# Optimization experiments

Measured on AMD Instinct MI355X. Metric: run time of the kernel, lower is better.

## Reference

```python
import jax, jax.numpy as jnp
import numpy as np

EPS = 0.01  # the module uses 1/sqrt(||x||^2 + 0.01) for cosine normalization


def setup_inputs() -> dict:
    key = jax.random.key(0)
    k1, k2, k3, k4, k5, k6 = jax.random.split(key, 6)
    B, L, L1, D = 512, 256, 256, 128
    sequence = jax.random.randint(k1, (B, L), 0, 10000, dtype=jnp.int32)
    last_sequence = jax.random.randint(k2, (B, L), 0, 2, dtype=jnp.int32)
    sequence_1 = jax.random.randint(k3, (B, L1), 0, 10000, dtype=jnp.int32)
    hist_1 = jax.random.normal(k4, (B, L, D), dtype=jnp.float32)
    hist_2 = jax.random.normal(k5, (B, L1, D), dtype=jnp.float32)
    W = jax.random.normal(k6, (D, D), dtype=jnp.float32) * (1.0 / np.sqrt(D))
    return {"sequence": sequence, "last_sequence": last_sequence,
            "sequence_1": sequence_1, "hist_1": hist_1, "hist_2": hist_2, "W": W}


def reference(sequence, last_sequence, sequence_1, hist_1, hist_2, W):
    # Masks: nonzero ids -> 1.0 (cast to bool then float in the original)
    m = (sequence != 0).astype(jnp.float32)        # [B, L]   key mask for self-attn
    m1 = (sequence_1 != 0).astype(jnp.float32)     # [B, L1]  key mask for cross-attn
    last = last_sequence.astype(jnp.float32)       # [B, L]   last-position indicator

    # --- self cosine-similarity attention over hist_1 ---
    # cos[b,i,j] = <hist_1[b,i], hist_1[b,j]> / (sqrt(||h_i||^2+eps) * sqrt(||h_j||^2+eps))
    dots = jnp.einsum('bid,bjd->bij', hist_1, hist_1)            # [B, L, L]
    inv = jax.lax.rsqrt(jnp.sum(hist_1 * hist_1, axis=-1) + EPS)  # [B, L]
    cos = dots * inv[:, :, None] * inv[:, None, :]
    # softmax-style weighting: exp(cos) masked over keys j (unnormalized exp, per original)
    w = jnp.exp(cos) * m[:, None, :]                             # [B, L, L]
    wsum = jnp.sum(w, axis=-1)                                   # [B, L]
    h_self = jnp.einsum('bij,bjd->bid', w, hist_1) / wsum[..., None]  # [B, L, D]

    # residual add, mask by query validity, then pool at the 'last' position
    h_all_add = (h_self + hist_1) * m[..., None]                 # [B, L, D]
    h_last = jnp.sum(h_all_add * last[..., None], axis=1)        # [B, D]

    # --- cross cosine-similarity attention: h_last attends over hist_2 ---
    dots2 = jnp.einsum('bkd,bd->bk', hist_2, h_last)             # [B, L1]
    inv2k = jax.lax.rsqrt(jnp.sum(hist_2 * hist_2, axis=-1) + EPS)  # [B, L1]
    inv2q = jax.lax.rsqrt(jnp.sum(h_last * h_last, axis=-1) + EPS)  # [B]
    cos2 = dots2 * inv2k * inv2q[:, None]
    w2 = jnp.exp(cos2) * m1                                      # [B, L1]
    h = jnp.einsum('bk,bkd->bd', w2, hist_2) / jnp.sum(w2, axis=-1, keepdims=True)

    out = jax.nn.relu(h @ W)                                     # [B, D]
    return out.reshape(-1, 1, W.shape[0])                        # [B, 1, hidden_num]
```

## Files before the change

### kernel.cpp

```cpp
#include <hip/hip_runtime.h>


using u16 = unsigned short;
using u32 = unsigned int;
typedef __attribute__((ext_vector_type(8))) short bf16x8;
typedef __attribute__((ext_vector_type(4))) float f32x4;
typedef __attribute__((ext_vector_type(4))) u32 u32x4;
typedef __attribute__((ext_vector_type(2))) u32 u32x2;

#define KST 136
#define TST 40
#define WSTR 40

__device__ __forceinline__ u16 f2bf(float f) {
  union { float f; u32 i; } v; v.f = f;
  u32 r = v.i + 0x7FFFu + ((v.i >> 16) & 1u);
  return (u16)(r >> 16);
}
__device__ __forceinline__ bf16x8 as_bf(u32x4 x) {
  union { u32x4 u; bf16x8 b; } c; c.u = x; return c.b;
}
__device__ __forceinline__ u32x4 pack_bf8(const float* p, float& ss) {
  const float4 a = *(const float4*)p;
  const float4 c = *(const float4*)(p + 4);
  ss += a.x*a.x + a.y*a.y + a.z*a.z + a.w*a.w
      + c.x*c.x + c.y*c.y + c.z*c.z + c.w*c.w;
  u32x4 v;
  v.x = (u32)f2bf(a.x) | ((u32)f2bf(a.y) << 16);
  v.y = (u32)f2bf(a.z) | ((u32)f2bf(a.w) << 16);
  v.z = (u32)f2bf(c.x) | ((u32)f2bf(c.y) << 16);
  v.w = (u32)f2bf(c.z) | ((u32)f2bf(c.w) << 16);
  return v;
}

__device__ __forceinline__ void stage_tile(u32x4 v, float ss, u16* kb, u16* tb,
                                           float* invt, int wv, int q, int m16) {
  const int row = wv * 4 + q;
  *(u32x4*)&kb[row * KST + m16 * 8] = v;
  ss += __shfl_xor(ss, 1); ss += __shfl_xor(ss, 2);
  ss += __shfl_xor(ss, 4); ss += __shfl_xor(ss, 8);
  if (m16 == 0) invt[row] = rsqrtf(ss + 0.01f);
  u32 w0 = v.x, w1 = v.y, w2 = v.z, w3 = v.w;
  {
    const int s1 = q & 1;
    u32 xa = s1 ? w0 : w1;
    u32 xb = s1 ? w2 : w3;
    xa = __shfl_xor(xa, 16);
    xb = __shfl_xor(xb, 16);
    if (s1) { w0 = xa; w2 = xb; } else { w1 = xa; w3 = xb; }
    const int s2 = q >> 1;
    u32 ya = s2 ? w0 : w2;
    u32 yb = s2 ? w1 : w3;
    ya = __shfl_xor(ya, 32);
    yb = __shfl_xor(yb, 32);
    if (s2) { w0 = ya; w1 = yb; } else { w2 = ya; w3 = yb; }
  }
  const int d0   = m16 * 8 + q * 2;
  const int base = wv * 4;
  u32x2 lo; lo.x = (w0 & 0xffffu) | (w1 << 16); lo.y = (w2 & 0xffffu) | (w3 << 16);
  u32x2 hi; hi.x = (w0 >> 16) | (w1 & 0xffff0000u); hi.y = (w2 >> 16) | (w3 & 0xffff0000u);
  *(u32x2*)&tb[d0 * TST + base]       = lo;
  *(u32x2*)&tb[(d0 + 1) * TST + base] = hi;
}

__launch_bounds__(512)
__global__ void itd_fused(const int* __restrict__ seq,
                          const int* __restrict__ lastseq,
                          const int* __restrict__ seq1,
                          const float* __restrict__ h1g,
                          const float* __restrict__ h2g,
                          const float* __restrict__ wg,
                          float* __restrict__ outg) {
  __shared__ u16 Kbuf[2][32 * KST];
  __shared__ u16 Tbuf[2][128 * TST];
  __shared__ u16 WST[8][2 * 16 * WSTR];
  __shared__ float MK[256], LM[256], HLacc[128], HH[128], INVt[2][32], SC[2];

  const int b    = blockIdx.x;
  const int t    = threadIdx.x;
  const int lane = t & 63;
  const int wv   = t >> 6;
  const int q    = lane >> 4;
  const int m16  = lane & 15;

  const float* h1b = h1g + (size_t)b * 32768;

  if (t < 128) HLacc[t] = 0.f;
  if (t < 256) {
    float m = (seq[b * 256 + t] != 0) ? 1.f : 0.f;
    MK[t] = m;
    LM[t] = m * (float)lastseq[b * 256 + t];
  }

  u32x4 av[2][4];
  float invi[2][4];
  #pragma unroll
  for (int rt = 0; rt < 2; ++rt) {
    const int i0 = wv * 32 + rt * 16;
    float ss = 0.f;
    #pragma unroll
    for (int s = 0; s < 4; ++s)
      av[rt][s] = pack_bf8(&h1b[(i0 + m16) * 128 + s * 32 + q * 8], ss);
    ss += __shfl_xor(ss, 16);
    ss += __shfl_xor(ss, 32);
    const float invrow = rsqrtf(ss + 0.01f);
    #pragma unroll
    for (int r = 0; r < 4; ++r) invi[rt][r] = __shfl(invrow, q * 4 + r);
  }

  const int srow = t >> 4;
  const int scol = (t & 15) * 8;
  {
    float ss = 0.f;
    u32x4 v0 = pack_bf8(&h1b[srow * 128 + scol], ss);
    stage_tile(v0, ss, Kbuf[0], Tbuf[0], INVt[0], wv, q, m16);
  }
  __syncthreads();

  const f32x4 fz = {0.f, 0.f, 0.f, 0.f};
  f32x4 acc[2][8];
  #pragma unroll
  for (int rt = 0; rt < 2; ++rt)
    #pragma unroll
    for (int dt = 0; dt < 8; ++dt) acc[rt][dt] = fz;
  float wpart[2][4] = {{0.f,0.f,0.f,0.f},{0.f,0.f,0.f,0.f}};
  u16* wst0 = &WST[wv][0];
  u16* wst1 = &WST[wv][16 * WSTR];

  for (int jt = 0; jt < 8; ++jt) {
    const int cur = jt & 1;
    float4 pfa, pfb;
    if (jt < 7) {
      const float* np = &h1b[(jt + 1) * 4096 + srow * 128 + scol];
      pfa = *(const float4*)np;
      pfb = *(const float4*)(np + 4);
    }

    f32x4 Sa[2] = {fz, fz}, Sb[2] = {fz, fz};
    const u16* kb = Kbuf[cur];
    #pragma unroll
    for (int s = 0; s < 4; ++s) {
      bf16x8 ba = *(const bf16x8*)&kb[m16 * KST + s * 32 + q * 8];
      bf16x8 bb = *(const bf16x8*)&kb[(16 + m16) * KST + s * 32 + q * 8];
      bf16x8 a0 = as_bf(av[0][s]);
      bf16x8 a1 = as_bf(av[1][s]);
      Sa[0] = __builtin_amdgcn_mfma_f32_16x16x32_bf16(a0, ba, Sa[0], 0, 0, 0);
      Sb[0] = __builtin_amdgcn_mfma_f32_16x16x32_bf16(a0, bb, Sb[0], 0, 0, 0);
      Sa[1] = __builtin_amdgcn_mfma_f32_16x16x32_bf16(a1, ba, Sa[1], 0, 0, 0);
      Sb[1] = __builtin_amdgcn_mfma_f32_16x16x32_bf16(a1, bb, Sb[1], 0, 0, 0);
    }
    const float invja = INVt[cur][m16];
    const float invjb = INVt[cur][16 + m16];
    const float mja = MK[jt * 32 + m16];
    const float mjb = MK[jt * 32 + 16 + m16];
    #pragma unroll
    for (int rt = 0; rt < 2; ++rt) {
      u16* wr = rt ? wst1 : wst0;
      #pragma unroll
      for (int r = 0; r < 4; ++r) {
        const float wa = __expf(Sa[rt][r] * (invi[rt][r] * invja)) * mja;
        const float wb = __expf(Sb[rt][r] * (invi[rt][r] * invjb)) * mjb;
        wpart[rt][r] += wa + wb;
        wr[(q * 4 + r) * WSTR + m16]      = f2bf(wa);
        wr[(q * 4 + r) * WSTR + 16 + m16] = f2bf(wb);
      }
    }
    __threadfence_block();
    const bf16x8 aw0 = *(const bf16x8*)&wst0[m16 * WSTR + q * 8];
    const bf16x8 aw1 = *(const bf16x8*)&wst1[m16 * WSTR + q * 8];
    const u16* tb = Tbuf[cur];
    #pragma unroll
    for (int dt = 0; dt < 8; ++dt) {
      const bf16x8 bt = *(const bf16x8*)&tb[(dt * 16 + m16) * TST + q * 8];
      acc[0][dt] = __builtin_amdgcn_mfma_f32_16x16x32_bf16(aw0, bt, acc[0][dt], 0, 0, 0);
      acc[1][dt] = __builtin_amdgcn_mfma_f32_16x16x32_bf16(aw1, bt, acc[1][dt], 0, 0, 0);
    }
    if (jt < 7) {
      float ss = pfa.x*pfa.x + pfa.y*pfa.y + pfa.z*pfa.z + pfa.w*pfa.w
               + pfb.x*pfb.x + pfb.y*pfb.y + pfb.z*pfb.z + pfb.w*pfb.w;
      u32x4 v;
      v.x = (u32)f2bf(pfa.x) | ((u32)f2bf(pfa.y) << 16);
      v.y = (u32)f2bf(pfa.z) | ((u32)f2bf(pfa.w) << 16);
      v.z = (u32)f2bf(pfb.x) | ((u32)f2bf(pfb.y) << 16);
      v.w = (u32)f2bf(pfb.z) | ((u32)f2bf(pfb.w) << 16);
      stage_tile(v, ss, Kbuf[cur ^ 1], Tbuf[cur ^ 1], INVt[cur ^ 1], wv, q, m16);
    }
    __syncthreads();
  }

  #pragma unroll
  for (int rt = 0; rt < 2; ++rt) {
    const int i0 = wv * 32 + rt * 16;
    float rws[4];
    #pragma unroll
    for (int r = 0; r < 4; ++r) {
      float s = wpart[rt][r];
      s += __shfl_xor(s, 1); s += __shfl_xor(s, 2);
      s += __shfl_xor(s, 4); s += __shfl_xor(s, 8);
      rws[r] = 1.f / s;
    }
    #pragma unroll
    for (int dt = 0; dt < 8; ++dt) {
      float v = 0.f;
      #pragma unroll
      for (int r = 0; r < 4; ++r)
        v += acc[rt][dt][r] * rws[r] * LM[i0 + q * 4 + r];
      v += __shfl_xor(v, 16);
      v += __shfl_xor(v, 32);
      if (q == 0) atomicAdd(&HLacc[dt * 16 + m16], v);
    }
  }

  {
    const int dd = t & 127, ig = t >> 7;
    float p = 0.f;
    #pragma unroll 8
    for (int n = 0; n < 64; ++n) {
      const int i = ig * 64 + n;
      p += LM[i] * h1b[i * 128 + dd];
    }
    ((float*)WST)[ig * 128 + dd] = p;
  }
  __syncthreads();
  if (t < 128) {
    const float* PSf = (const float*)WST;
    HLacc[t] += PSf[t] + PSf[128 + t] + PSf[256 + t] + PSf[384 + t];
  }
  __syncthreads();

  if (t < 64) {
    float s = HLacc[t] * HLacc[t] + HLacc[t + 64] * HLacc[t + 64];
    s += __shfl_xor(s, 1); s += __shfl_xor(s, 2); s += __shfl_xor(s, 4);
    s += __shfl_xor(s, 8); s += __shfl_xor(s, 16); s += __shfl_xor(s, 32);
    if (t == 0) SC[0] = rsqrtf(s + 0.01f);
  }
  if (t < 256) MK[t] = (seq1[b * 256 + t] != 0) ? 1.f : 0.f;
  __syncthreads();
  const float* h2b = h2g + (size_t)b * 32768;
  {
    const int k = t >> 1, half = t & 1;
    const float4* r = (const float4*)(h2b + k * 128 + half * 64);
    const float* hl = &HLacc[half * 64];
    float dot = 0.f, ss = 0.f;
    #pragma unroll
    for (int ii = 0; ii < 16; ++ii) {
      const float4 vv = r[ii];
      dot += vv.x * hl[ii*4] + vv.y * hl[ii*4+1] + vv.z * hl[ii*4+2] + vv.w * hl[ii*4+3];
      ss  += vv.x*vv.x + vv.y*vv.y + vv.z*vv.z + vv.w*vv.w;
    }
    dot += __shfl_xor(dot, 1);
    ss  += __shfl_xor(ss, 1);
    if (half == 0) LM[k] = __expf(dot * rsqrtf(ss + 0.01f) * SC[0]) * MK[k];
  }
  __syncthreads();
  if (t < 64) {
    float s = LM[t] + LM[t + 64] + LM[t + 128] + LM[t + 192];
    s += __shfl_xor(s, 1); s += __shfl_xor(s, 2); s += __shfl_xor(s, 4);
    s += __shfl_xor(s, 8); s += __shfl_xor(s, 16); s += __shfl_xor(s, 32);
    if (t == 0) SC[1] = s;
  }
  __syncthreads();
  {
    const int dd = t & 127, kg = t >> 7;
    float p = 0.f;
    #pragma unroll 8
    for (int n = 0; n < 64; ++n) {
      const int k = kg * 64 + n;
      p += LM[k] * h2b[k * 128 + dd];
    }
    ((float*)WST)[kg * 128 + dd] = p;
  }
  __syncthreads();
  if (t < 128) {
    const float* PSf = (const float*)WST;
    HH[t] = (PSf[t] + PSf[128 + t] + PSf[256 + t] + PSf[384 + t]) / SC[1];
  }
  __syncthreads();
  if (t < 128) {
    float o = 0.f;
    #pragma unroll 8
    for (int d = 0; d < 128; ++d)
      o += HH[d] * wg[d * 128 + t];
    outg[(size_t)b * 128 + t] = fmaxf(o, 0.f);
  }
}

extern "C" void kernel_launch(void* const* d_in, const int* in_sizes, int n_in,
                              void* d_out, int out_size, void* d_ws, size_t ws_size,
                              hipStream_t stream) {
  (void)in_sizes; (void)n_in; (void)d_ws; (void)ws_size; (void)out_size;
  const int*   seq     = (const int*)d_in[0];
  const int*   lastseq = (const int*)d_in[1];
  const int*   seq1    = (const int*)d_in[2];
  const float* h1      = (const float*)d_in[3];
  const float* h2      = (const float*)d_in[4];
  const float* w       = (const float*)d_in[5];
  float* out           = (float*)d_out;
  itd_fused<<<dim3(512), dim3(512), 0, stream>>>(seq, lastseq, seq1, h1, h2, w, out);
}
```

Before: 209.0 us.

## Split fused kernel into three kernels with per-batch query-half blocks

Splits the single 512-thread-per-batch kernel into three launches. The first is a self-attention kernel where two 256-thread blocks each handle half the queries of a batch. The second is a cross-attention kernel split over halves of the key range, and the third is a small output-projection kernel. The last-position pooling of hist_1 is folded into the K-tile staging loads, and a block fence is replaced by an explicit lgkmcnt wait. The aim is more blocks and better occupancy across CUs and less redundant global reading, at the cost of extra launches, workspace round-trips, and duplicate K/V staging per batch.

```diff
diff --git a/kernel.cpp b/kernel.cpp
--- a/kernel.cpp
+++ b/kernel.cpp
@@ -20,11 +20,7 @@
 __device__ __forceinline__ bf16x8 as_bf(u32x4 x) {
   union { u32x4 u; bf16x8 b; } c; c.u = x; return c.b;
 }
-__device__ __forceinline__ u32x4 pack_bf8(const float* p, float& ss) {
-  const float4 a = *(const float4*)p;
-  const float4 c = *(const float4*)(p + 4);
-  ss += a.x*a.x + a.y*a.y + a.z*a.z + a.w*a.w
-      + c.x*c.x + c.y*c.y + c.z*c.z + c.w*c.w;
+__device__ __forceinline__ u32x4 pack2(float4 a, float4 c) {
   u32x4 v;
   v.x = (u32)f2bf(a.x) | ((u32)f2bf(a.y) << 16);
   v.y = (u32)f2bf(a.z) | ((u32)f2bf(a.w) << 16);
@@ -32,10 +28,20 @@
   v.w = (u32)f2bf(c.z) | ((u32)f2bf(c.w) << 16);
   return v;
 }
+__device__ __forceinline__ float ssq2(float4 a, float4 c) {
+  return a.x*a.x + a.y*a.y + a.z*a.z + a.w*a.w
+       + c.x*c.x + c.y*c.y + c.z*c.z + c.w*c.w;
+}
+__device__ __forceinline__ u32x4 pack_bf8(const float* p, float& ss) {
+  const float4 a = *(const float4*)p;
+  const float4 c = *(const float4*)(p + 4);
+  ss += ssq2(a, c);
+  return pack2(a, c);
+}
 
 __device__ __forceinline__ void stage_tile(u32x4 v, float ss, u16* kb, u16* tb,
-                                           float* invt, int wv, int q, int m16) {
-  const int row = wv * 4 + q;
+                                           float* invt, int rowb, int q, int m16) {
+  const int row = rowb + q;
   *(u32x4*)&kb[row * KST + m16 * 8] = v;
   ss += __shfl_xor(ss, 1); ss += __shfl_xor(ss, 2);
   ss += __shfl_xor(ss, 4); ss += __shfl_xor(ss, 8);
@@ -55,48 +61,35 @@
     yb = __shfl_xor(yb, 32);
     if (s2) { w0 = ya; w1 = yb; } else { w2 = ya; w3 = yb; }
   }
-  const int d0   = m16 * 8 + q * 2;
-  const int base = wv * 4;
+  const int d0 = m16 * 8 + q * 2;
   u32x2 lo; lo.x = (w0 & 0xffffu) | (w1 << 16); lo.y = (w2 & 0xffffu) | (w3 << 16);
   u32x2 hi; hi.x = (w0 >> 16) | (w1 & 0xffff0000u); hi.y = (w2 >> 16) | (w3 & 0xffff0000u);
-  *(u32x2*)&tb[d0 * TST + base]       = lo;
-  *(u32x2*)&tb[(d0 + 1) * TST + base] = hi;
-}
-
-__launch_bounds__(512)
-__global__ void itd_fused(const int* __restrict__ seq,
-                          const int* __restrict__ lastseq,
-                          const int* __restrict__ seq1,
-                          const float* __restrict__ h1g,
-                          const float* __restrict__ h2g,
-                          const float* __restrict__ wg,
-                          float* __restrict__ outg) {
+  *(u32x2*)&tb[d0 * TST + rowb]       = lo;
+  *(u32x2*)&tb[(d0 + 1) * TST + rowb] = hi;
+}
+
+__global__ __launch_bounds__(256, 3)
+void k1_self(const int* __restrict__ seq, const int* __restrict__ lastseq,
+             const float* __restrict__ h1g, float* __restrict__ wsA) {
   __shared__ u16 Kbuf[2][32 * KST];
   __shared__ u16 Tbuf[2][128 * TST];
-  __shared__ u16 WST[8][2 * 16 * WSTR];
-  __shared__ float MK[256], LM[256], HLacc[128], HH[128], INVt[2][32], SC[2];
-
-  const int b    = blockIdx.x;
+  __shared__ u16 WST[4][2 * 16 * WSTR];
+  __shared__ float MK[256], LM[256], HLacc[128], INVt[2][32];
+
+  const int blk  = blockIdx.x;
+  const int b    = blk >> 1, half = blk & 1;
   const int t    = threadIdx.x;
-  const int lane = t & 63;
-  const int wv   = t >> 6;
-  const int q    = lane >> 4;
-  const int m16  = lane & 15;
-
+  const int lane = t & 63, wv = t >> 6, q = lane >> 4, m16 = lane & 15;
   const float* h1b = h1g + (size_t)b * 32768;
 
   if (t < 128) HLacc[t] = 0.f;
-  if (t < 256) {
-    float m = (seq[b * 256 + t] != 0) ? 1.f : 0.f;
-    MK[t] = m;
-    LM[t] = m * (float)lastseq[b * 256 + t];
-  }
-
-  u32x4 av[2][4];
-  float invi[2][4];
+  { float m = (seq[b * 256 + t] != 0) ? 1.f : 0.f;
+    MK[t] = m; LM[t] = m * (float)lastseq[b * 256 + t]; }
+
+  u32x4 av[2][4]; float invi[2][4];
   #pragma unroll
   for (int rt = 0; rt < 2; ++rt) {
-    const int i0 = wv * 32 + rt * 16;
+    const int i0 = half * 128 + wv * 32 + rt * 16;
     float ss = 0.f;
     #pragma unroll
     for (int s = 0; s < 4; ++s)
@@ -108,12 +101,24 @@
     for (int r = 0; r < 4; ++r) invi[rt][r] = __shfl(invrow, q * 4 + r);
   }
 
-  const int srow = t >> 4;
-  const int scol = (t & 15) * 8;
-  {
-    float ss = 0.f;
-    u32x4 v0 = pack_bf8(&h1b[srow * 128 + scol], ss);
-    stage_tile(v0, ss, Kbuf[0], Tbuf[0], INVt[0], wv, q, m16);
+  const int rl = t >> 4;
+  const int sc = (t & 15) * 8;
+  float racc[8] = {0.f,0.f,0.f,0.f,0.f,0.f,0.f,0.f};
+
+  __syncthreads();
+
+  #pragma unroll
+  for (int s = 0; s < 2; ++s) {
+    const int rloc = s * 16 + rl;
+    const float4 fa = *(const float4*)&h1b[rloc * 128 + sc];
+    const float4 fb = *(const float4*)&h1b[rloc * 128 + sc + 4];
+    if (half == 0) {
+      const float l = LM[rloc];
+      racc[0]+=l*fa.x; racc[1]+=l*fa.y; racc[2]+=l*fa.z; racc[3]+=l*fa.w;
+      racc[4]+=l*fb.x; racc[5]+=l*fb.y; racc[6]+=l*fb.z; racc[7]+=l*fb.w;
+    }
+    stage_tile(pack2(fa, fb), ssq2(fa, fb), Kbuf[0], Tbuf[0], INVt[0],
+               s * 16 + wv * 4, q, m16);
   }
   __syncthreads();
 
@@ -129,11 +134,13 @@
 
   for (int jt = 0; jt < 8; ++jt) {
     const int cur = jt & 1;
-    float4 pfa, pfb;
+    float4 pa0, pb0, pa1, pb1;
     if (jt < 7) {
-      const float* np = &h1b[(jt + 1) * 4096 + srow * 128 + scol];
-      pfa = *(const float4*)np;
-      pfb = *(const float4*)(np + 4);
+      const float* np = &h1b[(jt + 1) * 4096];
+      pa0 = *(const float4*)&np[rl * 128 + sc];
+      pb0 = *(const float4*)&np[rl * 128 + sc + 4];
+      pa1 = *(const float4*)&np[(16 + rl) * 128 + sc];
+      pb1 = *(const float4*)&np[(16 + rl) * 128 + sc + 4];
     }
 
     f32x4 Sa[2] = {fz, fz}, Sb[2] = {fz, fz};
@@ -165,7 +172,7 @@
         wr[(q * 4 + r) * WSTR + 16 + m16] = f2bf(wb);
       }
     }
-    __threadfence_block();
+    asm volatile("s_waitcnt lgkmcnt(0)" ::: "memory");
     const bf16x8 aw0 = *(const bf16x8*)&wst0[m16 * WSTR + q * 8];
     const bf16x8 aw1 = *(const bf16x8*)&wst1[m16 * WSTR + q * 8];
     const u16* tb = Tbuf[cur];
@@ -176,21 +183,25 @@
       acc[1][dt] = __builtin_amdgcn_mfma_f32_16x16x32_bf16(aw1, bt, acc[1][dt], 0, 0, 0);
     }
     if (jt < 7) {
-      float ss = pfa.x*pfa.x + pfa.y*pfa.y + pfa.z*pfa.z + pfa.w*pfa.w
-               + pfb.x*pfb.x + pfb.y*pfb.y + pfb.z*pfb.z + pfb.w*pfb.w;
-      u32x4 v;
-      v.x = (u32)f2bf(pfa.x) | ((u32)f2bf(pfa.y) << 16);
-      v.y = (u32)f2bf(pfa.z) | ((u32)f2bf(pfa.w) << 16);
-      v.z = (u32)f2bf(pfb.x) | ((u32)f2bf(pfb.y) << 16);
-      v.w = (u32)f2bf(pfb.z) | ((u32)f2bf(pfb.w) << 16);
-      stage_tile(v, ss, Kbuf[cur ^ 1], Tbuf[cur ^ 1], INVt[cur ^ 1], wv, q, m16);
+      if (half == 0) {
+        const float l0 = LM[(jt + 1) * 32 + rl];
+        const float l1 = LM[(jt + 1) * 32 + 16 + rl];
+        racc[0]+=l0*pa0.x+l1*pa1.x; racc[1]+=l0*pa0.y+l1*pa1.y;
+        racc[2]+=l0*pa0.z+l1*pa1.z; racc[3]+=l0*pa0.w+l1*pa1.w;
+        racc[4]+=l0*pb0.x+l1*pb1.x; racc[5]+=l0*pb0.y+l1*pb1.y;
+        racc[6]+=l0*pb0.z+l1*pb1.z; racc[7]+=l0*pb0.w+l1*pb1.w;
+      }
+      stage_tile(pack2(pa0, pb0), ssq2(pa0, pb0), Kbuf[cur ^ 1], Tbuf[cur ^ 1],
+                 INVt[cur ^ 1], wv * 4, q, m16);
+      stage_tile(pack2(pa1, pb1), ssq2(pa1, pb1), Kbuf[cur ^ 1], Tbuf[cur ^ 1],
+                 INVt[cur ^ 1], 16 + wv * 4, q, m16);
     }
     __syncthreads();
   }
 
   #pragma unroll
   for (int rt = 0; rt < 2; ++rt) {
-    const int i0 = wv * 32 + rt * 16;
+    const int i0 = half * 128 + wv * 32 + rt * 16;
     float rws[4];
     #pragma unroll
     for (int r = 0; r < 4; ++r) {
@@ -210,37 +221,46 @@
       if (q == 0) atomicAdd(&HLacc[dt * 16 + m16], v);
     }
   }
-
-  {
-    const int dd = t & 127, ig = t >> 7;
-    float p = 0.f;
-    #pragma unroll 8
-    for (int n = 0; n < 64; ++n) {
-      const int i = ig * 64 + n;
-      p += LM[i] * h1b[i * 128 + dd];
-    }
-    ((float*)WST)[ig * 128 + dd] = p;
+  __syncthreads();
+  if (half == 0) {
+    float* RES = (float*)WST;
+    float4 r0 = {racc[0], racc[1], racc[2], racc[3]};
+    float4 r1 = {racc[4], racc[5], racc[6], racc[7]};
+    *(float4*)&RES[rl * 128 + sc]     = r0;
+    *(float4*)&RES[rl * 128 + sc + 4] = r1;
   }
   __syncthreads();
   if (t < 128) {
-    const float* PSf = (const float*)WST;
-    HLacc[t] += PSf[t] + PSf[128 + t] + PSf[256 + t] + PSf[384 + t];
-  }
-  __syncthreads();
-
+    float vv = HLacc[t];
+    if (half == 0) {
+      const float* RES = (const float*)WST;
+      #pragma unroll
+      for (int r = 0; r < 16; ++r) vv += RES[r * 128 + t];
+    }
+    wsA[b * 256 + half * 128 + t] = vv;
+  }
+}
+
+__global__ __launch_bounds__(256)
+void k2_cross(const int* __restrict__ seq1, const float* __restrict__ h2g,
+              const float* __restrict__ wsA, float* __restrict__ wsB) {
+  __shared__ float HL[128], W2[128], PS[2][128], SCs[2];
+  const int blk = blockIdx.x, b = blk >> 1, kh = blk & 1;
+  const int t = threadIdx.x;
+  if (t < 128) HL[t] = wsA[b * 256 + t] + wsA[b * 256 + 128 + t];
+  __syncthreads();
   if (t < 64) {
-    float s = HLacc[t] * HLacc[t] + HLacc[t + 64] * HLacc[t + 64];
+    float s = HL[t] * HL[t] + HL[t + 64] * HL[t + 64];
     s += __shfl_xor(s, 1); s += __shfl_xor(s, 2); s += __shfl_xor(s, 4);
     s += __shfl_xor(s, 8); s += __shfl_xor(s, 16); s += __shfl_xor(s, 32);
-    if (t == 0) SC[0] = rsqrtf(s + 0.01f);
-  }
-  if (t < 256) MK[t] = (seq1[b * 256 + t] != 0) ? 1.f : 0.f;
+    if (t == 0) SCs[0] = rsqrtf(s + 0.01f);
+  }
   __syncthreads();
   const float* h2b = h2g + (size_t)b * 32768;
   {
-    const int k = t >> 1, half = t & 1;
-    const float4* r = (const float4*)(h2b + k * 128 + half * 64);
-    const float* hl = &HLacc[half * 64];
+    const int kl = t >> 1, h64 = t & 1;
+    const float4* r = (const float4*)(h2b + (size_t)(kh * 128 + kl) * 128 + h64 * 64);
+    const float* hl = &HL[h64 * 64];
     float dot = 0.f, ss = 0.f;
     #pragma unroll
     for (int ii = 0; ii < 16; ++ii) {
@@ -250,51 +270,60 @@
     }
     dot += __shfl_xor(dot, 1);
     ss  += __shfl_xor(ss, 1);
-    if (half == 0) LM[k] = __expf(dot * rsqrtf(ss + 0.01f) * SC[0]) * MK[k];
+    if (h64 == 0) {
+      const float mk = (seq1[b * 256 + kh * 128 + kl] != 0) ? 1.f : 0.f;
+      W2[kl] = __expf(dot * rsqrtf(ss + 0.01f) * SCs[0]) * mk;
+    }
   }
   __syncthreads();
   if (t < 64) {
-    float s = LM[t] + LM[t + 64] + LM[t + 128] + LM[t + 192];
+    float s = W2[t] + W2[t + 64];
     s += __shfl_xor(s, 1); s += __shfl_xor(s, 2); s += __shfl_xor(s, 4);
     s += __shfl_xor(s, 8); s += __shfl_xor(s, 16); s += __shfl_xor(s, 32);
-    if (t == 0) SC[1] = s;
-  }
-  __syncthreads();
+    if (t == 0) SCs[1] = s;
+  }
   {
-    const int dd = t & 127, kg = t >> 7;
+    const int d = t & 127, kg = t >> 7;
     float p = 0.f;
     #pragma unroll 8
-    for (int n = 0; n < 64; ++n) {
-      const int k = kg * 64 + n;
-      p += LM[k] * h2b[k * 128 + dd];
-    }
-    ((float*)WST)[kg * 128 + dd] = p;
-  }
-  __syncthreads();
-  if (t < 128) {
-    const float* PSf = (const float*)WST;
-    HH[t] = (PSf[t] + PSf[128 + t] + PSf[256 + t] + PSf[384 + t]) / SC[1];
-  }
-  __syncthreads();
-  if (t < 128) {
-    float o = 0.f;
-    #pragma unroll 8
-    for (int d = 0; d < 128; ++d)
-      o += HH[d] * wg[d * 128 + t];
-    outg[(size_t)b * 128 + t] = fmaxf(o, 0.f);
-  }
+    for (int n = 0; n < 64; ++n)
+      p += W2[kg * 64 + n] * h2b[(size_t)(kh * 128 + kg * 64 + n) * 128 + d];
+    PS[kg][d] = p;
+  }
+  __syncthreads();
+  if (t < 128) wsB[(b * 2 + kh) * 132 + t] = PS[0][t] + PS[1][t];
+  if (t == 128) wsB[(b * 2 + kh) * 132 + 128] = SCs[1];
+}
+
+__global__ __launch_bounds__(128)
+void k3_out(const float* __restrict__ wsB, const float* __restrict__ wg,
+            float* __restrict__ outg) {
+  __shared__ float HH[128];
+  const int b = blockIdx.x, t = threadIdx.x;
+  const float den = wsB[(b * 2) * 132 + 128] + wsB[(b * 2 + 1) * 132 + 128];
+  HH[t] = (wsB[(b * 2) * 132 + t] + wsB[(b * 2 + 1) * 132 + t]) / den;
+  __syncthreads();
+  float o = 0.f;
+  #pragma unroll 8
+  for (int d = 0; d < 128; ++d)
+    o += HH[d] * wg[d * 128 + t];
+  outg[(size_t)b * 128 + t] = fmaxf(o, 0.f);
 }
 
 extern "C" void kernel_launch(void* const* d_in, const int* in_sizes, int n_in,
                               void* d_out, int out_size, void* d_ws, size_t ws_size,
                               hipStream_t stream) {
-  (void)in_sizes; (void)n_in; (void)d_ws; (void)ws_size; (void)out_size;
+  (void)in_sizes; (void)n_in; (void)ws_size; (void)out_size;
   const int*   seq     = (const int*)d_in[0];
   const int*   lastseq = (const int*)d_in[1];
   const int*   seq1    = (const int*)d_in[2];
   const float* h1      = (const float*)d_in[3];
   const float* h2      = (const float*)d_in[4];
   const float* w       = (const float*)d_in[5];
-  float* out           = (float*)d_out;
-  itd_fused<<<dim3(512), dim3(512), 0, stream>>>(seq, lastseq, seq1, h1, h2, w, out);
-}
+  float* out = (float*)d_out;
+  float* wsA = (float*)d_ws;
+  float* wsB = wsA + 131072;
+  k1_self<<<dim3(1024), dim3(256), 0, stream>>>(seq, lastseq, h1, wsA);
+  k2_cross<<<dim3(1024), dim3(256), 0, stream>>>(seq1, h2, wsA, wsB);
+  k3_out<<<dim3(512), dim3(128), 0, stream>>>(wsB, w, out);
+}
```

Result: slower. 263.6 us (+26.1%).
